# Performance work log

Hardware: AMD Instinct MI355X
Metric: run time of the kernel (lower is better)

Reference implementation:

```python
import jax, jax.numpy as jnp
import numpy as np

N_NODES = 100000


def _gcn_layer(x, W, b, src, dst, dinv):
    # x: [N, din]; W: [din, dout]; src/dst: [E+N] (self-loops included); dinv: [N]
    h = x @ W                                   # [N, dout] small GEMM
    norm = dinv[src] * dinv[dst]                # [E+N]
    msg = h[src] * norm[:, None]                # [E+N, dout] gather
    out = jax.ops.segment_sum(msg, dst, num_segments=N_NODES)  # scatter-add
    return jax.nn.relu(out + b)


def setup_inputs() -> dict:
    key = jax.random.key(0)
    ks = jax.random.split(key, 8)
    d_in, d_h = 128, 128
    x = jax.random.normal(ks[0], (N_NODES, d_in), dtype=jnp.float32)
    edge_index = jax.random.randint(ks[1], (2, 1600000), 0, N_NODES, dtype=jnp.int64)
    def glorot(k, din, dout):
        lim = np.sqrt(6.0 / (din + dout)).astype(np.float32)
        return jax.random.uniform(k, (din, dout), jnp.float32, -lim, lim)
    W1 = glorot(ks[2], d_in, d_h); b1 = jnp.zeros((d_h,), jnp.float32)
    W2 = glorot(ks[3], d_h, d_h); b2 = jnp.zeros((d_h,), jnp.float32)
    W3 = glorot(ks[4], d_h, d_h); b3 = jnp.zeros((d_h,), jnp.float32)
    return {"x": x, "W1": W1, "b1": b1, "W2": W2, "b2": b2,
            "W3": W3, "b3": b3, "edge_index": edge_index}


def reference(x, W1, b1, W2, b2, W3, b3, edge_index):
    # GCNConv (Kipf & Welling): D^{-1/2}(A+I)D^{-1/2} X W + b, per layer, with ReLU.
    loop = jnp.arange(N_NODES, dtype=edge_index.dtype)
    src = jnp.concatenate([edge_index[0], loop])  # self-loops appended
    dst = jnp.concatenate([edge_index[1], loop])
    deg = jax.ops.segment_sum(jnp.ones_like(dst, dtype=x.dtype), dst,
                              num_segments=N_NODES)
    dinv = jnp.where(deg > 0, jax.lax.rsqrt(deg), 0.0)
    h = _gcn_layer(x, W1, b1, src, dst, dinv)
    h = _gcn_layer(h, W2, b2, src, dst, dinv)
    h = _gcn_layer(h, W3, b3, src, dst, dinv)
    return h
```

## Files before the change

### kernel.cpp

```cpp
#include <hip/hip_runtime.h>
#include <hip/hip_fp16.h>
#include <math.h>

#define NN 100000
#define DD 128
#define SCAN_CHUNK 2048

typedef short short8 __attribute__((ext_vector_type(8)));
typedef float f32x4 __attribute__((ext_vector_type(4)));

__global__ __launch_bounds__(256) void hist_rank_kernel(const int* __restrict__ dst, int E,
                                                        int* __restrict__ deg,
                                                        int* __restrict__ rank) {
    int i = blockIdx.x * 256 + threadIdx.x;
    int e = i * 4;
    if (e + 3 < E) {
        int4 d4 = ((const int4*)dst)[i];
        int4 r4;
        r4.x = atomicAdd(&deg[d4.x], 1);
        r4.y = atomicAdd(&deg[d4.y], 1);
        r4.z = atomicAdd(&deg[d4.z], 1);
        r4.w = atomicAdd(&deg[d4.w], 1);
        ((int4*)rank)[i] = r4;
    } else {
        for (; e < E; ++e) rank[e] = atomicAdd(&deg[dst[e]], 1);
    }
}

__global__ __launch_bounds__(256) void scan1_kernel(const int* __restrict__ deg,
                                                    int* __restrict__ chunkSum,
                                                    float* __restrict__ dinv, int n) {
    __shared__ int lds[256];
    int tid = threadIdx.x;
    int base = blockIdx.x * SCAN_CHUNK + tid * 8;
    int s = 0;
    #pragma unroll
    for (int j = 0; j < 8; ++j) {
        int idx = base + j;
        if (idx < n) {
            int d = deg[idx];
            s += d;
            dinv[idx] = rsqrtf((float)d + 1.0f);
        }
    }
    lds[tid] = s;
    __syncthreads();
    for (int d = 128; d > 0; d >>= 1) {
        if (tid < d) lds[tid] += lds[tid + d];
        __syncthreads();
    }
    if (tid == 0) chunkSum[blockIdx.x] = lds[0];
}

__global__ void scan2_kernel(int* __restrict__ chunkSum, int* __restrict__ chunkOff,
                             int nb, int* __restrict__ offsets) {
    __shared__ int lds[512];
    int tid = threadIdx.x;
    if (tid < nb) lds[tid] = chunkSum[tid];
    __syncthreads();
    if (tid == 0) {
        int run = 0;
        for (int i = 0; i < nb; ++i) {
            int v = lds[i];
            lds[i] = run;
            run += v;
        }
        offsets[NN] = run;
    }
    __syncthreads();
    if (tid < nb) chunkOff[tid] = lds[tid];
}

__global__ __launch_bounds__(256) void scan3_kernel(const int* __restrict__ deg,
                                                    const int* __restrict__ chunkOff,
                                                    int* __restrict__ offsets, int n) {
    __shared__ int lds[256];
    int tid = threadIdx.x;
    int base = blockIdx.x * SCAN_CHUNK + tid * 8;
    int v[8];
    int tsum = 0;
    #pragma unroll
    for (int j = 0; j < 8; ++j) {
        int idx = base + j;
        v[j] = (idx < n) ? deg[idx] : 0;
        tsum += v[j];
    }
    lds[tid] = tsum;
    __syncthreads();
    for (int d = 1; d < 256; d <<= 1) {
        int t = (tid >= d) ? lds[tid - d] : 0;
        __syncthreads();
        lds[tid] += t;
        __syncthreads();
    }
    int excl = lds[tid] - tsum;
    int off0 = chunkOff[blockIdx.x] + excl;
    int run = 0;
    #pragma unroll
    for (int j = 0; j < 8; ++j) {
        int idx = base + j;
        if (idx < n) offsets[idx] = off0 + run;
        run += v[j];
    }
}

__global__ __launch_bounds__(256) void fill_kernel(const int* __restrict__ src,
                                                   const int* __restrict__ dst,
                                                   const int* __restrict__ rank, int E,
                                                   const int* __restrict__ offsets,
                                                   int* __restrict__ csr) {
    int i = blockIdx.x * 256 + threadIdx.x;
    int e = i * 4;
    if (e + 3 < E) {
        int4 d4 = ((const int4*)dst)[i];
        int4 s4 = ((const int4*)src)[i];
        int4 r4 = ((const int4*)rank)[i];
        int o0 = offsets[d4.x];
        int o1 = offsets[d4.y];
        int o2 = offsets[d4.z];
        int o3 = offsets[d4.w];
        csr[o0 + r4.x] = s4.x;
        csr[o1 + r4.y] = s4.y;
        csr[o2 + r4.z] = s4.z;
        csr[o3 + r4.w] = s4.w;
    } else {
        for (; e < E; ++e) csr[offsets[dst[e]] + rank[e]] = src[e];
    }
}

__device__ __forceinline__ unsigned short f2bf(float f) {
    unsigned int u = __float_as_uint(f);
    unsigned int r = u + 0x7FFFu + ((u >> 16) & 1u);
    return (unsigned short)(r >> 16);
}

__device__ __forceinline__ void split8(const float* v, short8& hi, short8& lo) {
    #pragma unroll
    for (int j = 0; j < 8; ++j) {
        float f = v[j];
        unsigned short h = f2bf(f);
        float fl = f - __uint_as_float(((unsigned int)h) << 16);
        hi[j] = (short)h;
        lo[j] = (short)f2bf(fl);
    }
}

__global__ __launch_bounds__(256, 2) void gemm_norm_kernel(
    const float* __restrict__ X, const float* __restrict__ W,
    const float* __restrict__ dinv, __half* __restrict__ G)
{
    __shared__ uint4 whf[2048];
    __shared__ uint4 wlf[2048];

    const int tid  = threadIdx.x;
    const int base = blockIdx.x * 128;
    const int lane = tid & 63;
    const int wv   = tid >> 6;
    const int kg   = lane >> 4;
    const int mcol = lane & 15;

    #pragma unroll
    for (int p = 0; p < 8; ++p) {
        int i = tid + p * 256;
        int lane_e = i & 63;
        int ks = (i >> 6) & 3;
        int cf = i >> 8;
        int colb = cf * 16 + (lane_e & 15);
        int rowb = ks * 32 + (lane_e >> 4) * 8;
        float wvv[8];
        #pragma unroll
        for (int j = 0; j < 8; ++j) wvv[j] = W[(rowb + j) * DD + colb];
        short8 h, l;
        split8(wvv, h, l);
        union { short8 s; uint4 u; } ch, cl;
        ch.s = h; cl.s = l;
        whf[i] = ch.u;
        wlf[i] = cl.u;
    }

    short8 ah[2][4], al[2][4];
    #pragma unroll
    for (int rf = 0; rf < 2; ++rf) {
        int arow = base + wv * 32 + rf * 16 + mcol;
        if (arow >= NN) arow = NN - 1;
        const float* xr = X + (size_t)arow * DD;
        #pragma unroll
        for (int ks = 0; ks < 4; ++ks) {
            int k0 = ks * 32 + kg * 8;
            float av[8];
            *(float4*)&av[0] = *(const float4*)&xr[k0];
            *(float4*)&av[4] = *(const float4*)&xr[k0 + 4];
            split8(av, ah[rf][ks], al[rf][ks]);
        }
    }
    __syncthreads();

    #pragma unroll 1
    for (int cf = 0; cf < 8; ++cf) {
        f32x4 acc0 = {0.f, 0.f, 0.f, 0.f};
        f32x4 acc1 = {0.f, 0.f, 0.f, 0.f};
        #pragma unroll
        for (int ks = 0; ks < 4; ++ks) {
            union { uint4 u; short8 s; } bh, bl;
            bh.u = whf[(cf * 4 + ks) * 64 + lane];
            bl.u = wlf[(cf * 4 + ks) * 64 + lane];
            acc0 = __builtin_amdgcn_mfma_f32_16x16x32_bf16(ah[0][ks], bh.s, acc0, 0, 0, 0);
            acc0 = __builtin_amdgcn_mfma_f32_16x16x32_bf16(al[0][ks], bh.s, acc0, 0, 0, 0);
            acc0 = __builtin_amdgcn_mfma_f32_16x16x32_bf16(ah[0][ks], bl.s, acc0, 0, 0, 0);
            acc1 = __builtin_amdgcn_mfma_f32_16x16x32_bf16(ah[1][ks], bh.s, acc1, 0, 0, 0);
            acc1 = __builtin_amdgcn_mfma_f32_16x16x32_bf16(al[1][ks], bh.s, acc1, 0, 0, 0);
            acc1 = __builtin_amdgcn_mfma_f32_16x16x32_bf16(ah[1][ks], bl.s, acc1, 0, 0, 0);
        }
        #pragma unroll
        for (int rf = 0; rf < 2; ++rf) {
            const f32x4 acc = rf ? acc1 : acc0;
            int row0 = base + wv * 32 + rf * 16 + kg * 4;
            if (row0 < NN) {
                float dv[4];
                *(float4*)dv = *(const float4*)&dinv[row0];
                #pragma unroll
                for (int j = 0; j < 4; ++j) {
                    G[(size_t)(row0 + j) * DD + cf * 16 + mcol] =
                        __float2half(acc[j] * dv[j]);
                }
            }
        }
    }
}

__global__ __launch_bounds__(256) void agg_kernel(
    const __half* __restrict__ g, const float* __restrict__ dinv,
    const int* __restrict__ off, const int* __restrict__ csr,
    const float* __restrict__ bias, float* __restrict__ out)
{
    int node = (blockIdx.x * 256 + threadIdx.x) >> 6;
    if (node >= NN) return;
    int lane = threadIdx.x & 63;
    const __half2* __restrict__ g2 = (const __half2*)g;

    float2 acc0 = __half22float2(g2[node * 64 + lane]);
    float2 acc1 = make_float2(0.f, 0.f);

    int e = off[node], end = off[node + 1];
    int cnt = end - e;
    int e8end = e + (cnt & ~7);

    if (e < e8end) {
        int idx[8];
        #pragma unroll
        for (int j = 0; j < 8; ++j) idx[j] = csr[e + j];
        e += 8;
        for (; e < e8end; e += 8) {
            int nidx[8];
            #pragma unroll
            for (int j = 0; j < 8; ++j) nidx[j] = csr[e + j];
            #pragma unroll
            for (int j = 0; j < 8; j += 2) {
                float2 v0 = __half22float2(g2[idx[j] * 64 + lane]);
                float2 v1 = __half22float2(g2[idx[j + 1] * 64 + lane]);
                acc0.x += v0.x; acc0.y += v0.y;
                acc1.x += v1.x; acc1.y += v1.y;
            }
            #pragma unroll
            for (int j = 0; j < 8; ++j) idx[j] = nidx[j];
        }
        #pragma unroll
        for (int j = 0; j < 8; j += 2) {
            float2 v0 = __half22float2(g2[idx[j] * 64 + lane]);
            float2 v1 = __half22float2(g2[idx[j + 1] * 64 + lane]);
            acc0.x += v0.x; acc0.y += v0.y;
            acc1.x += v1.x; acc1.y += v1.y;
        }
    }
    for (; e < end; ++e) {
        float2 v = __half22float2(g2[csr[e] * 64 + lane]);
        acc0.x += v.x; acc0.y += v.y;
    }

    float di = dinv[node];
    float2 bb = ((const float2*)bias)[lane];
    float2 o;
    o.x = fmaxf(fmaf(acc0.x + acc1.x, di, bb.x), 0.f);
    o.y = fmaxf(fmaf(acc0.y + acc1.y, di, bb.y), 0.f);
    ((float2*)out)[node * 64 + lane] = o;
}

extern "C" void kernel_launch(void* const* d_in, const int* in_sizes, int n_in,
                              void* d_out, int out_size, void* d_ws, size_t ws_size,
                              hipStream_t stream)
{
    const float* x  = (const float*)d_in[0];
    const float* W1 = (const float*)d_in[1];
    const float* b1 = (const float*)d_in[2];
    const float* W2 = (const float*)d_in[3];
    const float* b2 = (const float*)d_in[4];
    const float* W3 = (const float*)d_in[5];
    const float* b3 = (const float*)d_in[6];
    const int*   ei = (const int*)d_in[7];

    const int E = in_sizes[7] / 2;
    const int* src = ei;
    const int* dst = ei + E;

    float* out = (float*)d_out;

    char* wsb = (char*)d_ws;
    size_t p = 0;
    int* deg      = (int*)(wsb + p); p += ((size_t)NN * 4 + 1023) & ~1023ull;
    int* offsets  = (int*)(wsb + p); p += ((size_t)(NN + 1) * 4 + 1023) & ~1023ull;
    int* chunkSum = (int*)(wsb + p); p += 4096;
    int* chunkOff = (int*)(wsb + p); p += 4096;
    int* csr      = (int*)(wsb + p); p += ((size_t)E * 4 + 1023) & ~1023ull;
    int* rank     = (int*)(wsb + p); p += ((size_t)E * 4 + 1023) & ~1023ull;
    float* dinv   = (float*)(wsb + p); p += ((size_t)NN * 4 + 1023) & ~1023ull;
    __half* g     = (__half*)(wsb + p); p += (size_t)NN * DD * 2;

    const int NB = (NN + SCAN_CHUNK - 1) / SCAN_CHUNK;

    hipMemsetAsync(deg, 0, (size_t)NN * 4, stream);
    hist_rank_kernel<<<(E / 4 + 256) / 256 + 1, 256, 0, stream>>>(dst, E, deg, rank);
    scan1_kernel<<<NB, 256, 0, stream>>>(deg, chunkSum, dinv, NN);
    scan2_kernel<<<1, 512, 0, stream>>>(chunkSum, chunkOff, NB, offsets);
    scan3_kernel<<<NB, 256, 0, stream>>>(deg, chunkOff, offsets, NN);
    fill_kernel<<<(E / 4 + 256) / 256 + 1, 256, 0, stream>>>(src, dst, rank, E, offsets, csr);

    const int gemm_grid = (NN + 127) / 128;
    const int agg_grid  = ((size_t)NN * 64 + 255) / 256;

    gemm_norm_kernel<<<gemm_grid, 256, 0, stream>>>(x, W1, dinv, g);
    agg_kernel<<<agg_grid, 256, 0, stream>>>(g, dinv, offsets, csr, b1, out);
    gemm_norm_kernel<<<gemm_grid, 256, 0, stream>>>(out, W2, dinv, g);
    agg_kernel<<<agg_grid, 256, 0, stream>>>(g, dinv, offsets, csr, b2, out);
    gemm_norm_kernel<<<gemm_grid, 256, 0, stream>>>(out, W3, dinv, g);
    agg_kernel<<<agg_grid, 256, 0, stream>>>(g, dinv, offsets, csr, b3, out);
}
```

Baseline: 413.0 us.

## Precompute W bf16 splits once and split aggregation across half-waves and column halves

Weight hi/lo bf16 splitting moves out of every GEMM block into a small pre-pass kernel per layer, so each GEMM block only copies pre-split tiles into shared memory instead of doing strided W reads and conversion. The aggregation kernel now gives each node two blocks, one per column half, and each wave's two 32-lane halves walk alternate edges before being combined with a cross-lane shuffle. This raises memory-level parallelism on the neighbor gathers, at the cost of reading the CSR index list twice and adding a reduction step.

```diff
diff --git a/kernel.cpp b/kernel.cpp
--- a/kernel.cpp
+++ b/kernel.cpp
@@ -145,8 +145,29 @@
     }
 }
 
+__global__ __launch_bounds__(256) void wsplit_kernel(const float* __restrict__ W,
+                                                     uint4* __restrict__ wh,
+                                                     uint4* __restrict__ wl) {
+    int i = blockIdx.x * 256 + threadIdx.x;
+    int lane_e = i & 63;
+    int ks = (i >> 6) & 3;
+    int cf = i >> 8;
+    int colb = cf * 16 + (lane_e & 15);
+    int rowb = ks * 32 + (lane_e >> 4) * 8;
+    float wvv[8];
+    #pragma unroll
+    for (int j = 0; j < 8; ++j) wvv[j] = W[(rowb + j) * DD + colb];
+    short8 h, l;
+    split8(wvv, h, l);
+    union { short8 s; uint4 u; } ch, cl;
+    ch.s = h; cl.s = l;
+    wh[i] = ch.u;
+    wl[i] = cl.u;
+}
+
 __global__ __launch_bounds__(256, 2) void gemm_norm_kernel(
-    const float* __restrict__ X, const float* __restrict__ W,
+    const float* __restrict__ X, const uint4* __restrict__ whg,
+    const uint4* __restrict__ wlg,
     const float* __restrict__ dinv, __half* __restrict__ G)
 {
     __shared__ uint4 whf[2048];
@@ -162,20 +183,8 @@
     #pragma unroll
     for (int p = 0; p < 8; ++p) {
         int i = tid + p * 256;
-        int lane_e = i & 63;
-        int ks = (i >> 6) & 3;
-        int cf = i >> 8;
-        int colb = cf * 16 + (lane_e & 15);
-        int rowb = ks * 32 + (lane_e >> 4) * 8;
-        float wvv[8];
-        #pragma unroll
-        for (int j = 0; j < 8; ++j) wvv[j] = W[(rowb + j) * DD + colb];
-        short8 h, l;
-        split8(wvv, h, l);
-        union { short8 s; uint4 u; } ch, cl;
-        ch.s = h; cl.s = l;
-        whf[i] = ch.u;
-        wlf[i] = cl.u;
+        whf[i] = whg[i];
+        wlf[i] = wlg[i];
     }
 
     short8 ah[2][4], al[2][4];
@@ -233,56 +242,80 @@
     const int* __restrict__ off, const int* __restrict__ csr,
     const float* __restrict__ bias, float* __restrict__ out)
 {
-    int node = (blockIdx.x * 256 + threadIdx.x) >> 6;
+    const int tid  = threadIdx.x;
+    const int wid  = tid >> 6;
+    const int lane = tid & 63;
+    const int sub  = lane >> 5;
+    const int cl   = lane & 31;
+    const int h    = blockIdx.x & 1;
+
+    int node = (int)(blockIdx.x >> 1) * 4 + wid;
     if (node >= NN) return;
-    int lane = threadIdx.x & 63;
+
     const __half2* __restrict__ g2 = (const __half2*)g;
-
-    float2 acc0 = __half22float2(g2[node * 64 + lane]);
-    float2 acc1 = make_float2(0.f, 0.f);
+    const int colb = h * 32 + cl;
+
+    float2 acc0 = make_float2(0.f, 0.f), acc1 = make_float2(0.f, 0.f);
+    if (sub == 0) acc0 = __half22float2(g2[node * 64 + colb]);
 
     int e = off[node], end = off[node + 1];
     int cnt = end - e;
-    int e8end = e + (cnt & ~7);
-
-    if (e < e8end) {
-        int idx[8];
-        #pragma unroll
-        for (int j = 0; j < 8; ++j) idx[j] = csr[e + j];
-        e += 8;
-        for (; e < e8end; e += 8) {
-            int nidx[8];
-            #pragma unroll
-            for (int j = 0; j < 8; ++j) nidx[j] = csr[e + j];
-            #pragma unroll
-            for (int j = 0; j < 8; j += 2) {
-                float2 v0 = __half22float2(g2[idx[j] * 64 + lane]);
-                float2 v1 = __half22float2(g2[idx[j + 1] * 64 + lane]);
-                acc0.x += v0.x; acc0.y += v0.y;
-                acc1.x += v1.x; acc1.y += v1.y;
-            }
-            #pragma unroll
-            for (int j = 0; j < 8; ++j) idx[j] = nidx[j];
-        }
-        #pragma unroll
-        for (int j = 0; j < 8; j += 2) {
-            float2 v0 = __half22float2(g2[idx[j] * 64 + lane]);
-            float2 v1 = __half22float2(g2[idx[j + 1] * 64 + lane]);
+    int pairs = cnt >> 1;
+    int np = pairs & ~3;
+
+    if (np) {
+        int i0 = csr[e + 0 + sub];
+        int i1 = csr[e + 2 + sub];
+        int i2 = csr[e + 4 + sub];
+        int i3 = csr[e + 6 + sub];
+        for (int p = 4; p < np; p += 4) {
+            int b0 = e + 2 * p + sub;
+            int j0 = csr[b0];
+            int j1 = csr[b0 + 2];
+            int j2 = csr[b0 + 4];
+            int j3 = csr[b0 + 6];
+            float2 v0 = __half22float2(g2[i0 * 64 + colb]);
+            float2 v1 = __half22float2(g2[i1 * 64 + colb]);
+            float2 v2 = __half22float2(g2[i2 * 64 + colb]);
+            float2 v3 = __half22float2(g2[i3 * 64 + colb]);
             acc0.x += v0.x; acc0.y += v0.y;
             acc1.x += v1.x; acc1.y += v1.y;
-        }
-    }
-    for (; e < end; ++e) {
-        float2 v = __half22float2(g2[csr[e] * 64 + lane]);
+            acc0.x += v2.x; acc0.y += v2.y;
+            acc1.x += v3.x; acc1.y += v3.y;
+            i0 = j0; i1 = j1; i2 = j2; i3 = j3;
+        }
+        float2 v0 = __half22float2(g2[i0 * 64 + colb]);
+        float2 v1 = __half22float2(g2[i1 * 64 + colb]);
+        float2 v2 = __half22float2(g2[i2 * 64 + colb]);
+        float2 v3 = __half22float2(g2[i3 * 64 + colb]);
+        acc0.x += v0.x; acc0.y += v0.y;
+        acc1.x += v1.x; acc1.y += v1.y;
+        acc0.x += v2.x; acc0.y += v2.y;
+        acc1.x += v3.x; acc1.y += v3.y;
+    }
+    for (int q = np; q < pairs; ++q) {
+        int s = csr[e + 2 * q + sub];
+        float2 v = __half22float2(g2[s * 64 + colb]);
         acc0.x += v.x; acc0.y += v.y;
     }
-
-    float di = dinv[node];
-    float2 bb = ((const float2*)bias)[lane];
-    float2 o;
-    o.x = fmaxf(fmaf(acc0.x + acc1.x, di, bb.x), 0.f);
-    o.y = fmaxf(fmaf(acc0.y + acc1.y, di, bb.y), 0.f);
-    ((float2*)out)[node * 64 + lane] = o;
+    if ((cnt & 1) && sub == 0) {
+        int s = csr[end - 1];
+        float2 v = __half22float2(g2[s * 64 + colb]);
+        acc0.x += v.x; acc0.y += v.y;
+    }
+
+    acc0.x += acc1.x; acc0.y += acc1.y;
+    acc0.x += __shfl_xor(acc0.x, 32, 64);
+    acc0.y += __shfl_xor(acc0.y, 32, 64);
+
+    if (sub == 0) {
+        float di = dinv[node];
+        float2 bb = ((const float2*)bias)[colb];
+        float2 o;
+        o.x = fmaxf(fmaf(acc0.x, di, bb.x), 0.f);
+        o.y = fmaxf(fmaf(acc0.y, di, bb.y), 0.f);
+        ((float2*)out)[node * 64 + colb] = o;
+    }
 }
 
 extern "C" void kernel_launch(void* const* d_in, const int* in_sizes, int n_in,
@@ -313,6 +346,8 @@
     int* csr      = (int*)(wsb + p); p += ((size_t)E * 4 + 1023) & ~1023ull;
     int* rank     = (int*)(wsb + p); p += ((size_t)E * 4 + 1023) & ~1023ull;
     float* dinv   = (float*)(wsb + p); p += ((size_t)NN * 4 + 1023) & ~1023ull;
+    uint4* wh     = (uint4*)(wsb + p); p += 3 * 2048 * sizeof(uint4);
+    uint4* wl     = (uint4*)(wsb + p); p += 3 * 2048 * sizeof(uint4);
     __half* g     = (__half*)(wsb + p); p += (size_t)NN * DD * 2;
 
     const int NB = (NN + SCAN_CHUNK - 1) / SCAN_CHUNK;
@@ -323,14 +358,17 @@
     scan2_kernel<<<1, 512, 0, stream>>>(chunkSum, chunkOff, NB, offsets);
     scan3_kernel<<<NB, 256, 0, stream>>>(deg, chunkOff, offsets, NN);
     fill_kernel<<<(E / 4 + 256) / 256 + 1, 256, 0, stream>>>(src, dst, rank, E, offsets, csr);
+    wsplit_kernel<<<8, 256, 0, stream>>>(W1, wh + 0 * 2048, wl + 0 * 2048);
+    wsplit_kernel<<<8, 256, 0, stream>>>(W2, wh + 1 * 2048, wl + 1 * 2048);
+    wsplit_kernel<<<8, 256, 0, stream>>>(W3, wh + 2 * 2048, wl + 2 * 2048);
 
     const int gemm_grid = (NN + 127) / 128;
-    const int agg_grid  = ((size_t)NN * 64 + 255) / 256;
-
-    gemm_norm_kernel<<<gemm_grid, 256, 0, stream>>>(x, W1, dinv, g);
+    const int agg_grid  = 2 * ((NN + 3) / 4);
+
+    gemm_norm_kernel<<<gemm_grid, 256, 0, stream>>>(x, wh + 0 * 2048, wl + 0 * 2048, dinv, g);
     agg_kernel<<<agg_grid, 256, 0, stream>>>(g, dinv, offsets, csr, b1, out);
-    gemm_norm_kernel<<<gemm_grid, 256, 0, stream>>>(out, W2, dinv, g);
+    gemm_norm_kernel<<<gemm_grid, 256, 0, stream>>>(out, wh + 1 * 2048, wl + 1 * 2048, dinv, g);
     agg_kernel<<<agg_grid, 256, 0, stream>>>(g, dinv, offsets, csr, b2, out);
-    gemm_norm_kernel<<<gemm_grid, 256, 0, stream>>>(out, W3, dinv, g);
+    gemm_norm_kernel<<<gemm_grid, 256, 0, stream>>>(out, W3 ? wh + 2 * 2048 : wh, wl + 2 * 2048, dinv, g);
     agg_kernel<<<agg_grid, 256, 0, stream>>>(g, dinv, offsets, csr, b3, out);
 }
```

After: 505.8 us. 1.22x slower.
